# Kernel optimization log

Measured on AMD Instinct MI355X. Metric: run time of the kernel, lower is better.

Reference implementation:

```python
import jax, jax.numpy as jnp
import numpy as np

N_NODES = 100000
N_EDGES = 3200000
NODE_F = 256
EDGE_F = 16
N_HEAD = 8
OUT_F = 256
NEG_SLOPE = 0.2
BN_EPS = 1e-5


def _seg_softmax(e, idx, num_segments):
    # numerically stable segment softmax over edges grouped by idx
    m = jax.ops.segment_max(e, idx, num_segments=num_segments)
    ex = jnp.exp(e - m[idx])
    s = jax.ops.segment_sum(ex, idx, num_segments=num_segments)
    return ex / s[idx]


def setup_inputs() -> dict:
    key = jax.random.key(0)
    ks = jax.random.split(key, 16)
    inp = {}
    inp["feat_src"] = jax.random.normal(ks[0], (N_NODES, NODE_F), jnp.float32)
    inp["feat_edge"] = jax.random.normal(ks[1], (N_EDGES, EDGE_F), jnp.float32)
    inp["src"] = jax.random.randint(ks[2], (N_EDGES,), 0, N_NODES, jnp.int32)
    inp["dst"] = jax.random.randint(ks[3], (N_EDGES,), 0, N_NODES, jnp.int32)
    def xav(k, fan_in, fan_out):
        # xavier_normal with relu gain sqrt(2)
        std = np.sqrt(2.0) * np.sqrt(2.0 / (fan_in + fan_out))
        return jax.random.normal(k, (fan_in, fan_out), jnp.float32) * std
    inp["W_prop_src"] = xav(ks[4], NODE_F, N_HEAD)
    inp["W_attn_src"] = xav(ks[5], NODE_F, N_HEAD)
    inp["W_attn_dst"] = xav(ks[6], NODE_F, N_HEAD)
    inp["W_attn_edge"] = xav(ks[7], EDGE_F, N_HEAD)
    inp["bn_gamma"] = jnp.ones((N_HEAD,), jnp.float32)
    inp["bn_beta"] = jnp.zeros((N_HEAD,), jnp.float32)
    inp["W_agg"] = xav(ks[8], N_HEAD, OUT_F)
    inp["b_agg"] = jnp.zeros((OUT_F,), jnp.float32)
    inp["W_apply_dst"] = xav(ks[9], NODE_F, OUT_F)
    inp["b_apply_dst"] = jnp.zeros((OUT_F,), jnp.float32)
    inp["W_apply"] = xav(ks[10], OUT_F, OUT_F)
    inp["b_apply"] = jnp.zeros((OUT_F,), jnp.float32)
    return inp


def reference(feat_src, feat_edge, src, dst, W_prop_src, W_attn_src, W_attn_dst,
              W_attn_edge, bn_gamma, bn_beta, W_agg, b_agg, W_apply_dst,
              b_apply_dst, W_apply, b_apply):
    leaky = lambda x: jnp.where(x >= 0, x, NEG_SLOPE * x)
    feat_dst = feat_src  # non-block graph
    feat_src_fc = feat_src @ W_prop_src            # [N, H]
    attn_src = feat_src @ W_attn_src               # [N, H]
    attn_dst = feat_dst @ W_attn_dst               # [N, H]
    attn_edge = feat_edge @ W_attn_edge            # [E, H]
    e = attn_src[src] + attn_dst[dst] + attn_edge  # [E, H]
    e = leaky(e)                                   # edge_att_actv = leaky_relu
    # dual softmax: geometric mean of dst- and src-normalized softmaxes
    a_dst = jnp.clip(_seg_softmax(e, dst, N_NODES), 1e-9)
    a_src = jnp.clip(_seg_softmax(e, src, N_NODES), 1e-9)
    a = jnp.sqrt(a_dst * a_src)                    # [E, H]
    msg_sum = jax.ops.segment_sum(feat_src_fc[src] * a, dst, num_segments=N_NODES)  # [N, H]
    # BatchNorm1d (training mode: batch statistics over nodes, biased var)
    mu = jnp.mean(msg_sum, axis=0)
    var = jnp.mean((msg_sum - mu) ** 2, axis=0)
    h = (msg_sum - mu) / jnp.sqrt(var + BN_EPS) * bn_gamma + bn_beta
    rst = h @ W_agg + b_agg                        # [N, OUT]
    rst = rst + feat_dst @ W_apply_dst + b_apply_dst
    rst = leaky(rst)
    rst = rst @ W_apply + b_apply
    return rst
```

## Files before the change

kernel.cpp:

```cpp
#include <hip/hip_runtime.h>

#define LRELU(x) ((x) >= 0.0f ? (x) : 0.2f * (x))

typedef __attribute__((ext_vector_type(8))) short short8;
typedef __attribute__((ext_vector_type(4))) float f32x4;

__device__ __forceinline__ unsigned short f2bf(float f) {
    union { float f; unsigned int u; } v; v.f = f;
    unsigned int u = v.u;
    u += 0x7FFFu + ((u >> 16) & 1u);
    return (unsigned short)(u >> 16);
}

__global__ __launch_bounds__(256) void k_node_tables(
    const float* __restrict__ feat,
    const float* __restrict__ Wp, const float* __restrict__ Was,
    const float* __restrict__ Wad,
    float* __restrict__ fc, float* __restrict__ as_t, float* __restrict__ ad_t,
    int N)
{
    __shared__ float Wl[3 * 2048];
    for (int i = threadIdx.x; i < 3 * 2048; i += 256) {
        float v;
        if (i < 2048)      v = Wp[i];
        else if (i < 4096) v = Was[i - 2048];
        else               v = Wad[i - 4096];
        Wl[i] = v;
    }
    __syncthreads();
    int gid = blockIdx.x * 256 + threadIdx.x;
    int n = gid >> 3, h = gid & 7;
    if (n >= N) return;
    const float4* f4 = (const float4*)(feat + (size_t)n * 256);
    float aP = 0.f, aS = 0.f, aD = 0.f;
#pragma unroll 8
    for (int k4 = 0; k4 < 64; ++k4) {
        float4 f = f4[k4];
        int b = k4 * 32 + h;
        aP += f.x * Wl[b]        + f.y * Wl[b + 8]        + f.z * Wl[b + 16]        + f.w * Wl[b + 24];
        aS += f.x * Wl[2048 + b] + f.y * Wl[2048 + b + 8] + f.z * Wl[2048 + b + 16] + f.w * Wl[2048 + b + 24];
        aD += f.x * Wl[4096 + b] + f.y * Wl[4096 + b + 8] + f.z * Wl[4096 + b + 16] + f.w * Wl[4096 + b + 24];
    }
    fc[gid] = aP; as_t[gid] = aS; ad_t[gid] = aD;
}

__device__ __forceinline__ float edge_ex(
    const float* __restrict__ feat_edge, const float* Wl,
    const float* __restrict__ as_t, const float* __restrict__ ad_t,
    int e, int h, int s, int d)
{
    const float4* fe = (const float4*)(feat_edge + (size_t)e * 16);
    float4 f0 = fe[0], f1 = fe[1], f2 = fe[2], f3 = fe[3];
    float ae = f0.x * Wl[h]      + f0.y * Wl[h + 8]   + f0.z * Wl[h + 16]  + f0.w * Wl[h + 24]
             + f1.x * Wl[h + 32] + f1.y * Wl[h + 40]  + f1.z * Wl[h + 48]  + f1.w * Wl[h + 56]
             + f2.x * Wl[h + 64] + f2.y * Wl[h + 72]  + f2.z * Wl[h + 80]  + f2.w * Wl[h + 88]
             + f3.x * Wl[h + 96] + f3.y * Wl[h + 104] + f3.z * Wl[h + 112] + f3.w * Wl[h + 120];
    float ev = as_t[s * 8 + h] + ad_t[d * 8 + h] + ae;
    ev = LRELU(ev);
    return __expf(ev);
}

__global__ __launch_bounds__(256) void k_edge1(
    const float* __restrict__ feat_edge,
    const int* __restrict__ src, const int* __restrict__ dst,
    const float* __restrict__ We,
    const float* __restrict__ as_t, const float* __restrict__ ad_t,
    float* __restrict__ sum_dst, float* __restrict__ sum_src, int E)
{
    __shared__ float Wl[128];
    if (threadIdx.x < 128) Wl[threadIdx.x] = We[threadIdx.x];
    __syncthreads();
    int gid = blockIdx.x * 256 + threadIdx.x;
    int e = gid >> 3, h = gid & 7;
    if (e >= E) return;
    int s = src[e], d = dst[e];
    float ex = edge_ex(feat_edge, Wl, as_t, ad_t, e, h, s, d);
    atomicAdd(&sum_dst[d * 8 + h], ex);
    atomicAdd(&sum_src[s * 8 + h], ex);
}

__global__ __launch_bounds__(256) void k_edge2(
    const float* __restrict__ feat_edge,
    const int* __restrict__ src, const int* __restrict__ dst,
    const float* __restrict__ We,
    const float* __restrict__ as_t, const float* __restrict__ ad_t,
    const float* __restrict__ sum_dst, const float* __restrict__ sum_src,
    const float* __restrict__ fc, float* __restrict__ msg, int E)
{
    __shared__ float Wl[128];
    if (threadIdx.x < 128) Wl[threadIdx.x] = We[threadIdx.x];
    __syncthreads();
    int gid = blockIdx.x * 256 + threadIdx.x;
    int e = gid >> 3, h = gid & 7;
    if (e >= E) return;
    int s = src[e], d = dst[e];
    float ex = edge_ex(feat_edge, Wl, as_t, ad_t, e, h, s, d);
    float a_d = fmaxf(ex / sum_dst[d * 8 + h], 1e-9f);
    float a_s = fmaxf(ex / sum_src[s * 8 + h], 1e-9f);
    float a = sqrtf(a_d * a_s);
    atomicAdd(&msg[d * 8 + h], fc[s * 8 + h] * a);
}

__global__ __launch_bounds__(256) void k_bn_stats(
    const float* __restrict__ msg, float* __restrict__ accum, int N)
{
    __shared__ float s1[8], s2[8];
    if (threadIdx.x < 8) { s1[threadIdx.x] = 0.f; s2[threadIdx.x] = 0.f; }
    __syncthreads();
    int h = threadIdx.x & 7;
    float a1 = 0.f, a2 = 0.f;
    int total = N * 8;
    for (int i = blockIdx.x * 256 + threadIdx.x; i < total; i += gridDim.x * 256) {
        float x = msg[i];
        a1 += x; a2 += x * x;
    }
    atomicAdd(&s1[h], a1);
    atomicAdd(&s2[h], a2);
    __syncthreads();
    if (threadIdx.x < 8) {
        atomicAdd(&accum[threadIdx.x], s1[threadIdx.x]);
        atomicAdd(&accum[8 + threadIdx.x], s2[threadIdx.x]);
    }
}

__global__ __launch_bounds__(256) void k_bn_apply(
    const float* __restrict__ msg, const float* __restrict__ accum,
    const float* __restrict__ gamma, const float* __restrict__ beta,
    float* __restrict__ h_t, int N)
{
    int i = blockIdx.x * 256 + threadIdx.x;
    if (i >= N * 8) return;
    int h = i & 7;
    float invN = 1.0f / (float)N;
    float mu = accum[h] * invN;
    float var = accum[8 + h] * invN - mu * mu;
    float rstd = rsqrtf(var + 1e-5f);
    h_t[i] = (msg[i] - mu) * rstd * gamma[h] + beta[h];
}

__global__ __launch_bounds__(256) void k_prep(
    const float* __restrict__ W1, const float* __restrict__ Wagg,
    const float* __restrict__ W2,
    const float* __restrict__ b_agg, const float* __restrict__ b1,
    const float* __restrict__ b2,
    unsigned short* __restrict__ B1t, unsigned short* __restrict__ B2t,
    float* __restrict__ bias1, float* __restrict__ bias2)
{
    int idx = blockIdx.x * 256 + threadIdx.x;
    if (idx < 73728) {
        int c = idx >> 13, rem = idx & 8191;
        int n = rem >> 5, k = rem & 31;
        float v;
        if (c < 8) v = W1[(c * 32 + k) * 256 + n];
        else       v = (k < 8) ? Wagg[k * 256 + n] : 0.f;
        B1t[idx] = f2bf(v);
    } else if (idx < 139264) {
        int j = idx - 73728;
        int c = j >> 13, rem = j & 8191;
        int n = rem >> 5, k = rem & 31;
        B2t[j] = f2bf(W2[(c * 32 + k) * 256 + n]);
    } else if (idx < 139520) {
        int n = idx - 139264;
        bias1[n] = b_agg[n] + b1[n];
    } else if (idx < 139776) {
        int n = idx - 139520;
        bias2[n] = b2[n];
    }
}

#define ASTRIDE 296

__global__ __launch_bounds__(256, 2) void k_fused_apply(
    const float* __restrict__ feat, const float* __restrict__ h_t,
    const unsigned short* __restrict__ B1t,
    const unsigned short* __restrict__ B2t,
    const float* __restrict__ bias1, const float* __restrict__ bias2,
    float* __restrict__ out, int N)
{
    __shared__ __align__(16) unsigned short As[64 * ASTRIDE];
    __shared__ __align__(16) unsigned short Bs[8192];

    int tid = threadIdx.x;
    int row0 = blockIdx.x * 64;

#pragma unroll
    for (int t = 0; t < 16; ++t) {
        int i = tid + t * 256;
        int r = i >> 6, k4 = i & 63;
        float4 f = make_float4(0.f, 0.f, 0.f, 0.f);
        if (row0 + r < N)
            f = ((const float4*)(feat + (size_t)(row0 + r) * 256))[k4];
        ushort4 b;
        b.x = f2bf(f.x); b.y = f2bf(f.y); b.z = f2bf(f.z); b.w = f2bf(f.w);
        *(ushort4*)&As[r * ASTRIDE + k4 * 4] = b;
    }
#pragma unroll
    for (int t = 0; t < 8; ++t) {
        int e = tid + t * 256;
        int r = e >> 5, c = e & 31;
        float v = 0.f;
        if (c < 8 && row0 + r < N) v = h_t[(size_t)(row0 + r) * 8 + c];
        As[r * ASTRIDE + 256 + c] = f2bf(v);
    }

    int wave = tid >> 6;
    int lane = tid & 63;
    int n16  = lane & 15;
    int quad = lane >> 4;
    int col0 = wave * 64;

    f32x4 acc[4][4];
#pragma unroll
    for (int rt = 0; rt < 4; ++rt)
#pragma unroll
        for (int ct = 0; ct < 4; ++ct)
            acc[rt][ct] = (f32x4){0.f, 0.f, 0.f, 0.f};

    for (int kc = 0; kc < 9; ++kc) {
        __syncthreads();
#pragma unroll
        for (int t = 0; t < 4; ++t) {
            int i = tid + t * 256;
            ((float4*)Bs)[i] = ((const float4*)(B1t + kc * 8192))[i];
        }
        __syncthreads();
        int kbase = kc * 32;
        short8 af[4], bf[4];
#pragma unroll
        for (int rt = 0; rt < 4; ++rt)
            af[rt] = *(const short8*)&As[(rt * 16 + n16) * ASTRIDE + kbase + quad * 8];
#pragma unroll
        for (int ct = 0; ct < 4; ++ct)
            bf[ct] = *(const short8*)&Bs[(col0 + ct * 16 + n16) * 32 + quad * 8];
#pragma unroll
        for (int rt = 0; rt < 4; ++rt)
#pragma unroll
            for (int ct = 0; ct < 4; ++ct)
                acc[rt][ct] = __builtin_amdgcn_mfma_f32_16x16x32_bf16(
                    af[rt], bf[ct], acc[rt][ct], 0, 0, 0);
    }

    float bi[4];
#pragma unroll
    for (int ct = 0; ct < 4; ++ct) bi[ct] = bias1[col0 + ct * 16 + n16];
    __syncthreads();
#pragma unroll
    for (int rt = 0; rt < 4; ++rt)
#pragma unroll
        for (int ct = 0; ct < 4; ++ct)
#pragma unroll
            for (int r = 0; r < 4; ++r) {
                float v = acc[rt][ct][r] + bi[ct];
                v = LRELU(v);
                int row = rt * 16 + quad * 4 + r;
                int col = col0 + ct * 16 + n16;
                As[row * ASTRIDE + col] = f2bf(v);
            }

#pragma unroll
    for (int rt = 0; rt < 4; ++rt)
#pragma unroll
        for (int ct = 0; ct < 4; ++ct)
            acc[rt][ct] = (f32x4){0.f, 0.f, 0.f, 0.f};

    for (int kc = 0; kc < 8; ++kc) {
        __syncthreads();
#pragma unroll
        for (int t = 0; t < 4; ++t) {
            int i = tid + t * 256;
            ((float4*)Bs)[i] = ((const float4*)(B2t + kc * 8192))[i];
        }
        __syncthreads();
        int kbase = kc * 32;
        short8 af[4], bf[4];
#pragma unroll
        for (int rt = 0; rt < 4; ++rt)
            af[rt] = *(const short8*)&As[(rt * 16 + n16) * ASTRIDE + kbase + quad * 8];
#pragma unroll
        for (int ct = 0; ct < 4; ++ct)
            bf[ct] = *(const short8*)&Bs[(col0 + ct * 16 + n16) * 32 + quad * 8];
#pragma unroll
        for (int rt = 0; rt < 4; ++rt)
#pragma unroll
            for (int ct = 0; ct < 4; ++ct)
                acc[rt][ct] = __builtin_amdgcn_mfma_f32_16x16x32_bf16(
                    af[rt], bf[ct], acc[rt][ct], 0, 0, 0);
    }

    float bi2[4];
#pragma unroll
    for (int ct = 0; ct < 4; ++ct) bi2[ct] = bias2[col0 + ct * 16 + n16];
#pragma unroll
    for (int rt = 0; rt < 4; ++rt)
#pragma unroll
        for (int r = 0; r < 4; ++r) {
            int row = row0 + rt * 16 + quad * 4 + r;
            if (row < N) {
#pragma unroll
                for (int ct = 0; ct < 4; ++ct) {
                    int col = col0 + ct * 16 + n16;
                    out[(size_t)row * 256 + col] = acc[rt][ct][r] + bi2[ct];
                }
            }
        }
}

extern "C" void kernel_launch(void* const* d_in, const int* in_sizes, int n_in,
                              void* d_out, int out_size, void* d_ws, size_t ws_size,
                              hipStream_t stream)
{
    const float* feat      = (const float*)d_in[0];
    const float* feat_edge = (const float*)d_in[1];
    const int*   src       = (const int*)d_in[2];
    const int*   dst       = (const int*)d_in[3];
    const float* W_prop    = (const float*)d_in[4];
    const float* W_as      = (const float*)d_in[5];
    const float* W_ad      = (const float*)d_in[6];
    const float* W_edge    = (const float*)d_in[7];
    const float* bn_gamma  = (const float*)d_in[8];
    const float* bn_beta   = (const float*)d_in[9];
    const float* W_agg     = (const float*)d_in[10];
    const float* b_agg     = (const float*)d_in[11];
    const float* W1        = (const float*)d_in[12];
    const float* b1        = (const float*)d_in[13];
    const float* W2        = (const float*)d_in[14];
    const float* b2        = (const float*)d_in[15];
    float* out = (float*)d_out;

    int N = in_sizes[0] / 256;
    int E = in_sizes[2];
    int N8 = N * 8;

    float* ws       = (float*)d_ws;
    float* sum_dst  = ws;
    float* sum_src  = sum_dst + N8;
    float* msg      = sum_src + N8;
    float* accum    = msg + N8;
    float* fc       = accum + 16;
    float* as_t     = fc + N8;
    float* ad_t     = as_t + N8;
    float* h_t      = ad_t + N8;
    float* bias1    = h_t + N8;
    float* bias2    = bias1 + 256;
    unsigned short* B1t = (unsigned short*)(bias2 + 256);
    unsigned short* B2t = B1t + 73728;

    hipMemsetAsync(d_ws, 0, (size_t)(3 * N8 + 16) * sizeof(float), stream);

    int gridN8 = (N8 + 255) / 256;
    int gridE8 = (E * 8 + 255) / 256;
    int gridF  = (N + 63) / 64;

    k_prep<<<546, 256, 0, stream>>>(W1, W_agg, W2, b_agg, b1, b2,
                                    B1t, B2t, bias1, bias2);
    k_node_tables<<<gridN8, 256, 0, stream>>>(feat, W_prop, W_as, W_ad,
                                              fc, as_t, ad_t, N);
    k_edge1<<<gridE8, 256, 0, stream>>>(feat_edge, src, dst, W_edge,
                                        as_t, ad_t, sum_dst, sum_src, E);
    k_edge2<<<gridE8, 256, 0, stream>>>(feat_edge, src, dst, W_edge,
                                        as_t, ad_t, sum_dst, sum_src,
                                        fc, msg, E);
    k_bn_stats<<<512, 256, 0, stream>>>(msg, accum, N);
    k_bn_apply<<<gridN8, 256, 0, stream>>>(msg, accum, bn_gamma, bn_beta, h_t, N);
    k_fused_apply<<<gridF, 256, 0, stream>>>(feat, h_t, B1t, B2t,
                                             bias1, bias2, out, N);
}
```

Before: 1.070 ms.

## Build CSR by dst/src per call and replace atomic edge passes with segmented reductions

Adds a per-call histogram, single-block scan and scatter to build dst-sorted and src-indexed edge lists. Edge exponentials are computed once, stored in bf16, and reduced per node by wave-level gathers instead of float atomics across two edge passes. BatchNorm apply is folded into the fused GEMM load. This adds three preprocessing kernels, a serial single-block scan, extra index traffic and bf16 rounding of the attention exponentials, and it falls back to the old path when the workspace is too small.

```diff
diff --git a/kernel.cpp b/kernel.cpp
--- a/kernel.cpp
+++ b/kernel.cpp
@@ -10,6 +10,11 @@
     unsigned int u = v.u;
     u += 0x7FFFu + ((u >> 16) & 1u);
     return (unsigned short)(u >> 16);
+}
+
+__device__ __forceinline__ float bf2f(unsigned short u) {
+    union { unsigned int u; float f; } v; v.u = ((unsigned int)u) << 16;
+    return v.f;
 }
 
 __global__ __launch_bounds__(256) void k_node_tables(
@@ -60,6 +65,131 @@
     return __expf(ev);
 }
 
+__global__ __launch_bounds__(256) void k_hist(
+    const int* __restrict__ src, const int* __restrict__ dst,
+    int* __restrict__ cnt, int N, int E)
+{
+    int e = blockIdx.x * 256 + threadIdx.x;
+    if (e >= E) return;
+    atomicAdd(&cnt[dst[e]], 1);
+    atomicAdd(&cnt[N + src[e]], 1);
+}
+
+__global__ __launch_bounds__(1024) void k_scan(
+    const int* __restrict__ cnt, int* __restrict__ off,
+    int* __restrict__ cur, int len)
+{
+    __shared__ int part[1024];
+    int t = threadIdx.x;
+    int C = (len + 1023) >> 10;
+    int b = t * C;
+    int e = b + C; if (e > len) e = len;
+    int s = 0;
+    for (int k = b; k < e; ++k) s += cnt[k];
+    part[t] = s;
+    __syncthreads();
+    for (int o = 1; o < 1024; o <<= 1) {
+        int v = (t >= o) ? part[t - o] : 0;
+        __syncthreads();
+        part[t] += v;
+        __syncthreads();
+    }
+    int run = (t == 0) ? 0 : part[t - 1];
+    for (int k = b; k < e; ++k) {
+        int c = cnt[k];
+        off[k] = run; cur[k] = run;
+        run += c;
+    }
+    if (t == 1023) off[len] = part[1023];
+}
+
+__global__ __launch_bounds__(256) void k_scatter(
+    const int* __restrict__ src, const int* __restrict__ dst,
+    int* __restrict__ cur,
+    int* __restrict__ ed_, int* __restrict__ sd_, int* __restrict__ dd_,
+    int* __restrict__ isrc_, int N, int E)
+{
+    int e = blockIdx.x * 256 + threadIdx.x;
+    if (e >= E) return;
+    int s = src[e], d = dst[e];
+    int i = atomicAdd(&cur[d], 1);
+    ed_[i] = e; sd_[i] = s; dd_[i] = d;
+    int j = atomicAdd(&cur[N + s], 1);
+    isrc_[j - E] = i;
+}
+
+__global__ __launch_bounds__(256) void k_ex(
+    const float* __restrict__ feat_edge, const float* __restrict__ We,
+    const int* __restrict__ ed_, const int* __restrict__ sd_,
+    const int* __restrict__ dd_,
+    const float* __restrict__ as_t, const float* __restrict__ ad_t,
+    unsigned short* __restrict__ exd, int E)
+{
+    __shared__ float Wl[128];
+    if (threadIdx.x < 128) Wl[threadIdx.x] = We[threadIdx.x];
+    __syncthreads();
+    int gid = blockIdx.x * 256 + threadIdx.x;
+    int i = gid >> 3, h = gid & 7;
+    if (i >= E) return;
+    int e = ed_[i], s = sd_[i], d = dd_[i];
+    float ex = edge_ex(feat_edge, Wl, as_t, ad_t, e, h, s, d);
+    exd[i * 8 + h] = f2bf(ex);
+}
+
+__global__ __launch_bounds__(256) void k_sums_src(
+    const unsigned short* __restrict__ exd, const int* __restrict__ isrc_,
+    const int* __restrict__ off, float* __restrict__ S_s, int N, int E)
+{
+    int wv = threadIdx.x >> 6;
+    int s = blockIdx.x * 4 + wv;
+    if (s >= N) return;
+    int lane = threadIdx.x & 63, g = lane >> 3;
+    int h = lane & 7;
+    int jb = off[N + s] - E, je = off[N + s + 1] - E;
+    float acc = 0.f;
+    for (int j = jb + g; j < je; j += 8) {
+        int i = isrc_[j];
+        acc += bf2f(exd[i * 8 + h]);
+    }
+    acc += __shfl_xor(acc, 8);
+    acc += __shfl_xor(acc, 16);
+    acc += __shfl_xor(acc, 32);
+    if (lane < 8) S_s[s * 8 + lane] = acc;
+}
+
+__global__ __launch_bounds__(256) void k_msg(
+    const unsigned short* __restrict__ exd, const int* __restrict__ sd_,
+    const int* __restrict__ off, const float* __restrict__ S_s,
+    const float* __restrict__ fc, float* __restrict__ msg, int N)
+{
+    int wv = threadIdx.x >> 6;
+    int d = blockIdx.x * 4 + wv;
+    if (d >= N) return;
+    int lane = threadIdx.x & 63, g = lane >> 3;
+    int h = lane & 7;
+    int db = off[d], de = off[d + 1];
+
+    float sdsum = 0.f;
+    for (int i = db + g; i < de; i += 8)
+        sdsum += bf2f(exd[i * 8 + h]);
+    sdsum += __shfl_xor(sdsum, 8);
+    sdsum += __shfl_xor(sdsum, 16);
+    sdsum += __shfl_xor(sdsum, 32);
+
+    float acc = 0.f;
+    for (int i = db + g; i < de; i += 8) {
+        int s = sd_[i];
+        float ex = bf2f(exd[i * 8 + h]);
+        float a_d = fmaxf(ex / sdsum, 1e-9f);
+        float a_s = fmaxf(ex / S_s[s * 8 + h], 1e-9f);
+        acc += fc[s * 8 + h] * sqrtf(a_d * a_s);
+    }
+    acc += __shfl_xor(acc, 8);
+    acc += __shfl_xor(acc, 16);
+    acc += __shfl_xor(acc, 32);
+    if (lane < 8) msg[d * 8 + lane] = acc;
+}
+
 __global__ __launch_bounds__(256) void k_edge1(
     const float* __restrict__ feat_edge,
     const int* __restrict__ src, const int* __restrict__ dst,
@@ -121,21 +251,6 @@
         atomicAdd(&accum[threadIdx.x], s1[threadIdx.x]);
         atomicAdd(&accum[8 + threadIdx.x], s2[threadIdx.x]);
     }
-}
-
-__global__ __launch_bounds__(256) void k_bn_apply(
-    const float* __restrict__ msg, const float* __restrict__ accum,
-    const float* __restrict__ gamma, const float* __restrict__ beta,
-    float* __restrict__ h_t, int N)
-{
-    int i = blockIdx.x * 256 + threadIdx.x;
-    if (i >= N * 8) return;
-    int h = i & 7;
-    float invN = 1.0f / (float)N;
-    float mu = accum[h] * invN;
-    float var = accum[8 + h] * invN - mu * mu;
-    float rstd = rsqrtf(var + 1e-5f);
-    h_t[i] = (msg[i] - mu) * rstd * gamma[h] + beta[h];
 }
 
 __global__ __launch_bounds__(256) void k_prep(
@@ -171,7 +286,9 @@
 #define ASTRIDE 296
 
 __global__ __launch_bounds__(256, 2) void k_fused_apply(
-    const float* __restrict__ feat, const float* __restrict__ h_t,
+    const float* __restrict__ feat, const float* __restrict__ msg,
+    const float* __restrict__ accum,
+    const float* __restrict__ gamma, const float* __restrict__ beta,
     const unsigned short* __restrict__ B1t,
     const unsigned short* __restrict__ B2t,
     const float* __restrict__ bias1, const float* __restrict__ bias2,
@@ -199,7 +316,13 @@
         int e = tid + t * 256;
         int r = e >> 5, c = e & 31;
         float v = 0.f;
-        if (c < 8 && row0 + r < N) v = h_t[(size_t)(row0 + r) * 8 + c];
+        if (c < 8 && row0 + r < N) {
+            float invN = 1.0f / (float)N;
+            float mu = accum[c] * invN;
+            float var = accum[8 + c] * invN - mu * mu;
+            float rstd = rsqrtf(var + 1e-5f);
+            v = (msg[(size_t)(row0 + r) * 8 + c] - mu) * rstd * gamma[c] + beta[c];
+        }
         As[r * ASTRIDE + 256 + c] = f2bf(v);
     }
 
@@ -331,37 +454,81 @@
     int E = in_sizes[2];
     int N8 = N * 8;
 
-    float* ws       = (float*)d_ws;
-    float* sum_dst  = ws;
-    float* sum_src  = sum_dst + N8;
-    float* msg      = sum_src + N8;
-    float* accum    = msg + N8;
-    float* fc       = accum + 16;
-    float* as_t     = fc + N8;
-    float* ad_t     = as_t + N8;
-    float* h_t      = ad_t + N8;
-    float* bias1    = h_t + N8;
-    float* bias2    = bias1 + 256;
-    unsigned short* B1t = (unsigned short*)(bias2 + 256);
-    unsigned short* B2t = B1t + 73728;
-
-    hipMemsetAsync(d_ws, 0, (size_t)(3 * N8 + 16) * sizeof(float), stream);
-
-    int gridN8 = (N8 + 255) / 256;
-    int gridE8 = (E * 8 + 255) / 256;
-    int gridF  = (N + 63) / 64;
-
-    k_prep<<<546, 256, 0, stream>>>(W1, W_agg, W2, b_agg, b1, b2,
-                                    B1t, B2t, bias1, bias2);
-    k_node_tables<<<gridN8, 256, 0, stream>>>(feat, W_prop, W_as, W_ad,
-                                              fc, as_t, ad_t, N);
-    k_edge1<<<gridE8, 256, 0, stream>>>(feat_edge, src, dst, W_edge,
-                                        as_t, ad_t, sum_dst, sum_src, E);
-    k_edge2<<<gridE8, 256, 0, stream>>>(feat_edge, src, dst, W_edge,
-                                        as_t, ad_t, sum_dst, sum_src,
-                                        fc, msg, E);
-    k_bn_stats<<<512, 256, 0, stream>>>(msg, accum, N);
-    k_bn_apply<<<gridN8, 256, 0, stream>>>(msg, accum, bn_gamma, bn_beta, h_t, N);
-    k_fused_apply<<<gridF, 256, 0, stream>>>(feat, h_t, B1t, B2t,
-                                             bias1, bias2, out, N);
-}
+    int gridN8    = (N8 + 255) / 256;
+    int gridE     = (E + 255) / 256;
+    int gridE8    = (E * 8 + 255) / 256;
+    int gridNode4 = (N + 3) / 4;
+    int gridF     = (N + 63) / 64;
+
+    char* base = (char*)d_ws;
+    size_t o = 0;
+    auto take = [&](size_t bytes) -> char* {
+        char* p = base + o;
+        o = (o + bytes + 63) & ~(size_t)63;
+        return p;
+    };
+    int*   cnt   = (int*)  take((size_t)2 * N * sizeof(int));
+    float* accum = (float*)take(16 * sizeof(float));
+    int*   off   = (int*)  take((size_t)(2 * N + 1) * sizeof(int));
+    int*   cur   = (int*)  take((size_t)2 * N * sizeof(int));
+    float* S_s   = (float*)take((size_t)N8 * sizeof(float));
+    float* msg   = (float*)take((size_t)N8 * sizeof(float));
+    float* fc    = (float*)take((size_t)N8 * sizeof(float));
+    float* as_t  = (float*)take((size_t)N8 * sizeof(float));
+    float* ad_t  = (float*)take((size_t)N8 * sizeof(float));
+    float* bias1 = (float*)take(256 * sizeof(float));
+    float* bias2 = (float*)take(256 * sizeof(float));
+    unsigned short* B1t = (unsigned short*)take(73728 * sizeof(unsigned short));
+    unsigned short* B2t = (unsigned short*)take(65536 * sizeof(unsigned short));
+    int*   ed_   = (int*)  take((size_t)E * sizeof(int));
+    int*   sd_   = (int*)  take((size_t)E * sizeof(int));
+    int*   dd_   = (int*)  take((size_t)E * sizeof(int));
+    int*   isrc_ = (int*)  take((size_t)E * sizeof(int));
+    unsigned short* exd = (unsigned short*)take((size_t)E * 8 * sizeof(unsigned short));
+    size_t need_csr = o;
+
+    if (ws_size >= need_csr) {
+        hipMemsetAsync(d_ws, 0, (size_t)2 * N * sizeof(int) + 64, stream);
+        k_prep<<<546, 256, 0, stream>>>(W1, W_agg, W2, b_agg, b1, b2,
+                                        B1t, B2t, bias1, bias2);
+        k_node_tables<<<gridN8, 256, 0, stream>>>(feat, W_prop, W_as, W_ad,
+                                                  fc, as_t, ad_t, N);
+        k_hist<<<gridE, 256, 0, stream>>>(src, dst, cnt, N, E);
+        k_scan<<<1, 1024, 0, stream>>>(cnt, off, cur, 2 * N);
+        k_scatter<<<gridE, 256, 0, stream>>>(src, dst, cur, ed_, sd_, dd_, isrc_, N, E);
+        k_ex<<<gridE8, 256, 0, stream>>>(feat_edge, W_edge, ed_, sd_, dd_,
+                                         as_t, ad_t, exd, E);
+        k_sums_src<<<gridNode4, 256, 0, stream>>>(exd, isrc_, off, S_s, N, E);
+        k_msg<<<gridNode4, 256, 0, stream>>>(exd, sd_, off, S_s, fc, msg, N);
+        k_bn_stats<<<512, 256, 0, stream>>>(msg, accum, N);
+        k_fused_apply<<<gridF, 256, 0, stream>>>(feat, msg, accum, bn_gamma, bn_beta,
+                                                 B1t, B2t, bias1, bias2, out, N);
+    } else {
+        float* ws       = (float*)d_ws;
+        float* sum_dst  = ws;
+        float* sum_src  = sum_dst + N8;
+        float* msgF     = sum_src + N8;
+        float* accumF   = msgF + N8;
+        float* fcF      = accumF + 16;
+        float* asF      = fcF + N8;
+        float* adF      = asF + N8;
+        float* bias1F   = adF + N8;
+        float* bias2F   = bias1F + 256;
+        unsigned short* B1tF = (unsigned short*)(bias2F + 256);
+        unsigned short* B2tF = B1tF + 73728;
+
+        hipMemsetAsync(d_ws, 0, (size_t)(3 * N8 + 16) * sizeof(float), stream);
+        k_prep<<<546, 256, 0, stream>>>(W1, W_agg, W2, b_agg, b1, b2,
+                                        B1tF, B2tF, bias1F, bias2F);
+        k_node_tables<<<gridN8, 256, 0, stream>>>(feat, W_prop, W_as, W_ad,
+                                                  fcF, asF, adF, N);
+        k_edge1<<<gridE8, 256, 0, stream>>>(feat_edge, src, dst, W_edge,
+                                            asF, adF, sum_dst, sum_src, E);
+        k_edge2<<<gridE8, 256, 0, stream>>>(feat_edge, src, dst, W_edge,
+                                            asF, adF, sum_dst, sum_src,
+                                            fcF, msgF, E);
+        k_bn_stats<<<512, 256, 0, stream>>>(msgF, accumF, N);
+        k_fused_apply<<<gridF, 256, 0, stream>>>(feat, msgF, accumF, bn_gamma, bn_beta,
+                                                 B1tF, B2tF, bias1F, bias2F, out, N);
+    }
+}
```

New measurement: 2.031 ms. +89.8%, slower.

## Cache edge exponentials in bf16, use packed bf16 atomics, fuse BN apply

Applied to the files above, without the earlier changes.

The first edge pass now stores exp(e) per edge-head as bf16 and accumulates the softmax denominators with packed bf16 atomic adds, two heads per atomic. This halves the atomic count and the size of the sum tables. The second edge pass reads the cached values instead of re-reading edge features and recomputing attention logits. Batch-norm normalization is folded into the final GEMM's A-tile load, so the separate apply kernel and its h_t buffer are dropped. The cost is precision: the denominators are accumulated in bf16 over about 32 edges per node, which may lose accuracy, and the bf16 cache adds a 51 MB write and read.

```diff
diff --git a/kernel.cpp b/kernel.cpp
--- a/kernel.cpp
+++ b/kernel.cpp
@@ -10,6 +10,16 @@
     unsigned int u = v.u;
     u += 0x7FFFu + ((u >> 16) & 1u);
     return (unsigned short)(u >> 16);
+}
+
+__device__ __forceinline__ float bf2f(unsigned short u) {
+    union { unsigned int u; float f; } v; v.u = ((unsigned int)u) << 16;
+    return v.f;
+}
+
+__device__ __forceinline__ void atomic_pk_add_bf16(unsigned short* p, unsigned int pk) {
+    asm volatile("global_atomic_pk_add_bf16 %0, %1, off"
+                 :: "v"(p), "v"(pk) : "memory");
 }
 
 __global__ __launch_bounds__(256) void k_node_tables(
@@ -65,7 +75,9 @@
     const int* __restrict__ src, const int* __restrict__ dst,
     const float* __restrict__ We,
     const float* __restrict__ as_t, const float* __restrict__ ad_t,
-    float* __restrict__ sum_dst, float* __restrict__ sum_src, int E)
+    unsigned short* __restrict__ sum_dst_bf,
+    unsigned short* __restrict__ sum_src_bf,
+    unsigned short* __restrict__ exd, int E)
 {
     __shared__ float Wl[128];
     if (threadIdx.x < 128) Wl[threadIdx.x] = We[threadIdx.x];
@@ -75,30 +87,33 @@
     if (e >= E) return;
     int s = src[e], d = dst[e];
     float ex = edge_ex(feat_edge, Wl, as_t, ad_t, e, h, s, d);
-    atomicAdd(&sum_dst[d * 8 + h], ex);
-    atomicAdd(&sum_src[s * 8 + h], ex);
+    unsigned short exb = f2bf(ex);
+    exd[gid] = exb;
+    float exn = __shfl_xor(ex, 1);
+    if ((h & 1) == 0) {
+        unsigned int pk = (unsigned int)exb | ((unsigned int)f2bf(exn) << 16);
+        atomic_pk_add_bf16(sum_dst_bf + d * 8 + h, pk);
+        atomic_pk_add_bf16(sum_src_bf + s * 8 + h, pk);
+    }
 }
 
 __global__ __launch_bounds__(256) void k_edge2(
-    const float* __restrict__ feat_edge,
+    const unsigned short* __restrict__ exd,
     const int* __restrict__ src, const int* __restrict__ dst,
-    const float* __restrict__ We,
-    const float* __restrict__ as_t, const float* __restrict__ ad_t,
-    const float* __restrict__ sum_dst, const float* __restrict__ sum_src,
+    const unsigned short* __restrict__ sum_dst_bf,
+    const unsigned short* __restrict__ sum_src_bf,
     const float* __restrict__ fc, float* __restrict__ msg, int E)
 {
-    __shared__ float Wl[128];
-    if (threadIdx.x < 128) Wl[threadIdx.x] = We[threadIdx.x];
-    __syncthreads();
     int gid = blockIdx.x * 256 + threadIdx.x;
     int e = gid >> 3, h = gid & 7;
     if (e >= E) return;
     int s = src[e], d = dst[e];
-    float ex = edge_ex(feat_edge, Wl, as_t, ad_t, e, h, s, d);
-    float a_d = fmaxf(ex / sum_dst[d * 8 + h], 1e-9f);
-    float a_s = fmaxf(ex / sum_src[s * 8 + h], 1e-9f);
-    float a = sqrtf(a_d * a_s);
-    atomicAdd(&msg[d * 8 + h], fc[s * 8 + h] * a);
+    float ex = bf2f(exd[gid]);
+    float Sd = bf2f(sum_dst_bf[d * 8 + h]);
+    float Ss = bf2f(sum_src_bf[s * 8 + h]);
+    float a_d = fmaxf(ex / Sd, 1e-9f);
+    float a_s = fmaxf(ex / Ss, 1e-9f);
+    atomicAdd(&msg[d * 8 + h], fc[s * 8 + h] * sqrtf(a_d * a_s));
 }
 
 __global__ __launch_bounds__(256) void k_bn_stats(
@@ -121,21 +136,6 @@
         atomicAdd(&accum[threadIdx.x], s1[threadIdx.x]);
         atomicAdd(&accum[8 + threadIdx.x], s2[threadIdx.x]);
     }
-}
-
-__global__ __launch_bounds__(256) void k_bn_apply(
-    const float* __restrict__ msg, const float* __restrict__ accum,
-    const float* __restrict__ gamma, const float* __restrict__ beta,
-    float* __restrict__ h_t, int N)
-{
-    int i = blockIdx.x * 256 + threadIdx.x;
-    if (i >= N * 8) return;
-    int h = i & 7;
-    float invN = 1.0f / (float)N;
-    float mu = accum[h] * invN;
-    float var = accum[8 + h] * invN - mu * mu;
-    float rstd = rsqrtf(var + 1e-5f);
-    h_t[i] = (msg[i] - mu) * rstd * gamma[h] + beta[h];
 }
 
 __global__ __launch_bounds__(256) void k_prep(
@@ -171,7 +171,9 @@
 #define ASTRIDE 296
 
 __global__ __launch_bounds__(256, 2) void k_fused_apply(
-    const float* __restrict__ feat, const float* __restrict__ h_t,
+    const float* __restrict__ feat, const float* __restrict__ msg,
+    const float* __restrict__ accum,
+    const float* __restrict__ gamma, const float* __restrict__ beta,
     const unsigned short* __restrict__ B1t,
     const unsigned short* __restrict__ B2t,
     const float* __restrict__ bias1, const float* __restrict__ bias2,
@@ -199,7 +201,13 @@
         int e = tid + t * 256;
         int r = e >> 5, c = e & 31;
         float v = 0.f;
-        if (c < 8 && row0 + r < N) v = h_t[(size_t)(row0 + r) * 8 + c];
+        if (c < 8 && row0 + r < N) {
+            float invN = 1.0f / (float)N;
+            float mu = accum[c] * invN;
+            float var = accum[8 + c] * invN - mu * mu;
+            float rstd = rsqrtf(var + 1e-5f);
+            v = (msg[(size_t)(row0 + r) * 8 + c] - mu) * rstd * gamma[c] + beta[c];
+        }
         As[r * ASTRIDE + 256 + c] = f2bf(v);
     }
 
@@ -331,21 +339,29 @@
     int E = in_sizes[2];
     int N8 = N * 8;
 
-    float* ws       = (float*)d_ws;
-    float* sum_dst  = ws;
-    float* sum_src  = sum_dst + N8;
-    float* msg      = sum_src + N8;
-    float* accum    = msg + N8;
-    float* fc       = accum + 16;
-    float* as_t     = fc + N8;
-    float* ad_t     = as_t + N8;
-    float* h_t      = ad_t + N8;
-    float* bias1    = h_t + N8;
-    float* bias2    = bias1 + 256;
-    unsigned short* B1t = (unsigned short*)(bias2 + 256);
-    unsigned short* B2t = B1t + 73728;
-
-    hipMemsetAsync(d_ws, 0, (size_t)(3 * N8 + 16) * sizeof(float), stream);
+    char* base = (char*)d_ws;
+    size_t o = 0;
+    auto take = [&](size_t bytes) -> char* {
+        char* p = base + o;
+        o = (o + bytes + 63) & ~(size_t)63;
+        return p;
+    };
+    unsigned short* sum_dst_bf = (unsigned short*)take((size_t)N8 * 2);
+    unsigned short* sum_src_bf = (unsigned short*)take((size_t)N8 * 2);
+    float* msg   = (float*)take((size_t)N8 * sizeof(float));
+    float* accum = (float*)take(16 * sizeof(float));
+    size_t zero_bytes = o;
+    float* fc    = (float*)take((size_t)N8 * sizeof(float));
+    float* as_t  = (float*)take((size_t)N8 * sizeof(float));
+    float* ad_t  = (float*)take((size_t)N8 * sizeof(float));
+    float* bias1 = (float*)take(256 * sizeof(float));
+    float* bias2 = (float*)take(256 * sizeof(float));
+    unsigned short* B1t = (unsigned short*)take(73728 * sizeof(unsigned short));
+    unsigned short* B2t = (unsigned short*)take(65536 * sizeof(unsigned short));
+    unsigned short* exd = (unsigned short*)take((size_t)E * 8 * sizeof(unsigned short));
+    (void)ws_size;
+
+    hipMemsetAsync(d_ws, 0, zero_bytes, stream);
 
     int gridN8 = (N8 + 255) / 256;
     int gridE8 = (E * 8 + 255) / 256;
@@ -356,12 +372,11 @@
     k_node_tables<<<gridN8, 256, 0, stream>>>(feat, W_prop, W_as, W_ad,
                                               fc, as_t, ad_t, N);
     k_edge1<<<gridE8, 256, 0, stream>>>(feat_edge, src, dst, W_edge,
-                                        as_t, ad_t, sum_dst, sum_src, E);
-    k_edge2<<<gridE8, 256, 0, stream>>>(feat_edge, src, dst, W_edge,
-                                        as_t, ad_t, sum_dst, sum_src,
+                                        as_t, ad_t, sum_dst_bf, sum_src_bf,
+                                        exd, E);
+    k_edge2<<<gridE8, 256, 0, stream>>>(exd, src, dst, sum_dst_bf, sum_src_bf,
                                         fc, msg, E);
     k_bn_stats<<<512, 256, 0, stream>>>(msg, accum, N);
-    k_bn_apply<<<gridN8, 256, 0, stream>>>(msg, accum, bn_gamma, bn_beta, h_t, N);
-    k_fused_apply<<<gridF, 256, 0, stream>>>(feat, h_t, B1t, B2t,
-                                             bias1, bias2, out, N);
-}
+    k_fused_apply<<<gridF, 256, 0, stream>>>(feat, msg, accum, bn_gamma, bn_beta,
+                                             B1t, B2t, bias1, bias2, out, N);
+}
```

Measured after the change: 974.0 us. 1.1x faster.
